# Performance work log

Hardware: AMD Instinct MI355X
Metric: run time of the kernel (lower is better)

## Reference

```python
import jax, jax.numpy as jnp
import numpy as np

N = 50000      # nodes
E = 800000     # edges (before self-loops)
IN_DIM = 128
HID = 64
OUT = 32
HEADS = 8
BN_EPS = 1e-5
NEG_SLOPE = 0.2  # PyG GATConv default


def setup_inputs() -> dict:
    key = jax.random.key(0)
    ks = jax.random.split(key, 24)
    g = lambda k, shape, fan_in: (jax.random.normal(k, shape, jnp.float32) / np.sqrt(fan_in))
    return {
        "x": jax.random.normal(ks[0], (N, IN_DIM), jnp.float32),
        "edge_index": jax.random.randint(ks[1], (2, E), 0, N, dtype=jnp.int64),
        # GCN1
        "gcn1_w": g(ks[2], (IN_DIM, HID), IN_DIM),
        "gcn1_b": jnp.zeros((HID,), jnp.float32),
        # BN1 (eval mode running stats)
        "bn1_gamma": jnp.ones((HID,), jnp.float32),
        "bn1_beta": jnp.zeros((HID,), jnp.float32),
        "bn1_mean": 0.1 * jax.random.normal(ks[3], (HID,), jnp.float32),
        "bn1_var": 0.5 + jax.random.uniform(ks[4], (HID,), jnp.float32),
        # GAT1: heads=8, per-head out=HID, concat=False -> mean over heads
        "gat1_w": g(ks[5], (HID, HEADS * HID), HID),
        "gat1_asrc": g(ks[6], (HEADS, HID), HID),
        "gat1_adst": g(ks[7], (HEADS, HID), HID),
        "gat1_b": jnp.zeros((HID,), jnp.float32),
        # GCN2
        "gcn2_w": g(ks[8], (HID, HID), HID),
        "gcn2_b": jnp.zeros((HID,), jnp.float32),
        # BN2
        "bn2_gamma": jnp.ones((HID,), jnp.float32),
        "bn2_beta": jnp.zeros((HID,), jnp.float32),
        "bn2_mean": 0.1 * jax.random.normal(ks[9], (HID,), jnp.float32),
        "bn2_var": 0.5 + jax.random.uniform(ks[10], (HID,), jnp.float32),
        # GAT2: heads=8, per-head out=OUT, concat=False
        "gat2_w": g(ks[11], (HID, HEADS * OUT), HID),
        "gat2_asrc": g(ks[12], (HEADS, OUT), OUT),
        "gat2_adst": g(ks[13], (HEADS, OUT), OUT),
        "gat2_b": jnp.zeros((OUT,), jnp.float32),
    }


def _gcn(x, src, dst, w, b, n):
    # PyG GCNConv: x @ W, symmetric norm with self-loops (src/dst already include them)
    h = x @ w
    deg = jax.ops.segment_sum(jnp.ones(src.shape[0], x.dtype), dst, num_segments=n)
    dinv = jnp.where(deg > 0, jax.lax.rsqrt(jnp.maximum(deg, 1.0)), 0.0)
    coef = dinv[src] * dinv[dst]                     # [E']
    out = jax.ops.segment_sum(coef[:, None] * h[src], dst, num_segments=n)
    return out + b


def _gat(x, src, dst, w, a_src, a_dst, b, n, heads, ch):
    # PyG GATConv (concat=False): mean over heads, softmax over incoming edges per dst
    h = (x @ w).reshape(n, heads, ch)                # [N,H,C]
    es = jnp.einsum('nhc,hc->nh', h, a_src)          # alpha_src per node
    ed = jnp.einsum('nhc,hc->nh', h, a_dst)
    e = jax.nn.leaky_relu(es[src] + ed[dst], NEG_SLOPE)  # [E',H]
    m = jax.ops.segment_max(e, dst, num_segments=n)
    m = jnp.where(jnp.isfinite(m), m, 0.0)
    ex = jnp.exp(e - m[dst])
    denom = jax.ops.segment_sum(ex, dst, num_segments=n)
    alpha = ex / (denom[dst] + 1e-16)                # [E',H]
    out = jnp.zeros((n, ch), x.dtype)
    for hd in range(heads):  # fixed small head loop keeps peak edge memory at [E',C]
        msg = alpha[:, hd, None] * h[src, hd]        # [E',C]
        out = out + jax.ops.segment_sum(msg, dst, num_segments=n)
    return out / heads + b


def _bn_eval(x, gamma, beta, mean, var):
    return (x - mean) * jax.lax.rsqrt(var + BN_EPS) * gamma + beta


def reference(x, edge_index,
              gcn1_w, gcn1_b, bn1_gamma, bn1_beta, bn1_mean, bn1_var,
              gat1_w, gat1_asrc, gat1_adst, gat1_b,
              gcn2_w, gcn2_b, bn2_gamma, bn2_beta, bn2_mean, bn2_var,
              gat2_w, gat2_asrc, gat2_adst, gat2_b):
    n = x.shape[0]
    loops = jnp.arange(n, dtype=edge_index.dtype)
    src = jnp.concatenate([edge_index[0], loops])    # self-loops (PyG default)
    dst = jnp.concatenate([edge_index[1], loops])

    h = _gcn(x, src, dst, gcn1_w, gcn1_b, n)
    h = jax.nn.relu(_bn_eval(h, bn1_gamma, bn1_beta, bn1_mean, bn1_var))
    h = jax.nn.relu(_gat(h, src, dst, gat1_w, gat1_asrc, gat1_adst, gat1_b, n, HEADS, HID))
    h = _gcn(h, src, dst, gcn2_w, gcn2_b, n)
    h = jax.nn.relu(_bn_eval(h, bn2_gamma, bn2_beta, bn2_mean, bn2_var))
    h = _gat(h, src, dst, gat2_w, gat2_asrc, gat2_adst, gat2_b, n, HEADS, OUT)
    return jax.nn.log_softmax(h, axis=1)
```

## Files before the change

kernel.cpp:

```cpp
#include <hip/hip_runtime.h>
#include <hip/hip_bf16.h>

#define NN 50000
#define NE 800000
#define IND 128
#define NH 8
#define EBLK 256
#define EPB 3125
#define NBUK 391
#define NBUKP 392
#define GH (NBUKP * EBLK)

typedef __hip_bfloat16 bf16;
typedef __attribute__((ext_vector_type(8))) short short8;
typedef __attribute__((ext_vector_type(8))) __bf16 bf16x8;
typedef __attribute__((ext_vector_type(4))) float floatx4;
typedef __attribute__((ext_vector_type(2))) float floatx2;

static __device__ __forceinline__ short f2bf_bits(float f) {
    unsigned u = __float_as_uint(f);
    u = (u + 0x7fffu + ((u >> 16) & 1u)) >> 16;
    return (short)u;
}
static __device__ __forceinline__ float bf2f(bf16 v) { return __bfloat162float(v); }
static __device__ __forceinline__ floatx2 up2(unsigned av) {
    floatx2 r;
    r.x = __uint_as_float(av << 16);
    r.y = __uint_as_float(av & 0xffff0000u);
    return r;
}
static __device__ __forceinline__ unsigned pk2(float a, float b) {
    return (unsigned)(unsigned short)f2bf_bits(a) | ((unsigned)(unsigned short)f2bf_bits(b) << 16);
}

__global__ __launch_bounds__(256) void bin_count_kernel(const int* __restrict__ edst,
        int* __restrict__ ghist) {
    __shared__ int h[NBUKP];
    const int tid = threadIdx.x, blk = blockIdx.x;
    for (int b = tid; b < NBUKP; b += 256) h[b] = 0;
    __syncthreads();
    const int e0 = blk * EPB;
    for (int e = e0 + tid; e < e0 + EPB; e += 256)
        atomicAdd(&h[edst[e] >> 7], 1);
    __syncthreads();
    for (int b = tid; b < NBUKP; b += 256)
        ghist[b * EBLK + blk] = h[b];
}
__global__ __launch_bounds__(256) void scang1_kernel(const int* __restrict__ src,
        int* __restrict__ pre, int* __restrict__ bsum, int n) {
    __shared__ int sh[256];
    const int tid = threadIdx.x;
    const int idx = blockIdx.x * 256 + tid;
    int c = (idx < n) ? src[idx] : 0;
    sh[tid] = c; __syncthreads();
    int val = c;
#pragma unroll
    for (int off = 1; off < 256; off <<= 1) {
        int t = (tid >= off) ? sh[tid - off] : 0;
        __syncthreads();
        val += t; sh[tid] = val;
        __syncthreads();
    }
    if (idx < n) pre[idx] = val - c;
    if (tid == 255) bsum[blockIdx.x] = val;
}
__global__ __launch_bounds__(512) void scang2_kernel(int* __restrict__ bsum, int nb) {
    __shared__ int sh[512];
    const int tid = threadIdx.x;
    int v = (tid < nb) ? bsum[tid] : 0;
    sh[tid] = v; __syncthreads();
    int val = v;
#pragma unroll
    for (int off = 1; off < 512; off <<= 1) {
        int t = (tid >= off) ? sh[tid - off] : 0;
        __syncthreads();
        val += t; sh[tid] = val;
        __syncthreads();
    }
    if (tid < nb) bsum[tid] = val - v;
}
__global__ __launch_bounds__(256) void bin_scatter_kernel(const int* __restrict__ esrc,
        const int* __restrict__ edst, const int* __restrict__ gpre,
        const int* __restrict__ gbsum, unsigned* __restrict__ ebuf) {
    __shared__ int cur[NBUKP];
    const int tid = threadIdx.x, blk = blockIdx.x;
    for (int b = tid; b < NBUKP; b += 256) {
        int i = b * EBLK + blk;
        cur[b] = gpre[i] + gbsum[i >> 8];
    }
    __syncthreads();
    const int e0 = blk * EPB;
    for (int e = e0 + tid; e < e0 + EPB; e += 256) {
        int d = edst[e], s = esrc[e];
        int pos = atomicAdd(&cur[d >> 7], 1);
        ebuf[pos] = ((unsigned)(d & 127) << 16) | (unsigned)s;
    }
}
__global__ __launch_bounds__(256) void bucket_finalize_kernel(const unsigned* __restrict__ ebuf,
        const int* __restrict__ gpre, const int* __restrict__ gbsum,
        int* __restrict__ rowptr, float* __restrict__ dinv, int* __restrict__ csrc) {
    __shared__ int lh[128], lcur[128], sc[256];
    const int bu = blockIdx.x, tid = threadIdx.x;
    const int seg_beg = gpre[bu * EBLK] + gbsum[bu];
    const int seg_end = gpre[(bu + 1) * EBLK] + gbsum[bu + 1];
    if (tid < 128) lh[tid] = 0;
    __syncthreads();
    for (int i = seg_beg + tid; i < seg_end; i += 256)
        atomicAdd(&lh[ebuf[i] >> 16], 1);
    __syncthreads();
    int c = (tid < 128) ? lh[tid] : 0;
    sc[tid] = c; __syncthreads();
    int val = c;
#pragma unroll
    for (int off = 1; off < 256; off <<= 1) {
        int t = (tid >= off) ? sc[tid - off] : 0;
        __syncthreads();
        val += t; sc[tid] = val;
        __syncthreads();
    }
    int excl = val - c;
    if (tid < 128) {
        lcur[tid] = excl;
        int node = bu * 128 + tid;
        if (node < NN) {
            rowptr[node] = seg_beg + excl;
            dinv[node] = rsqrtf((float)c + 1.f);
        }
    }
    if (bu == 0 && tid == 0) rowptr[NN] = NE;
    __syncthreads();
    for (int i = seg_beg + tid; i < seg_end; i += 256) {
        unsigned u = ebuf[i];
        int pos = atomicAdd(&lcur[u >> 16], 1);
        csrc[seg_beg + pos] = (int)(u & 0xffffu);
    }
}

__global__ __launch_bounds__(256) void prep_all_kernel(
        const float* __restrict__ gcn1_w, const float* __restrict__ gcn2_w,
        const float* __restrict__ gat1_w, const float* __restrict__ gat2_w,
        const float* __restrict__ as1, const float* __restrict__ ad1,
        const float* __restrict__ as2, const float* __restrict__ ad2,
        bf16* __restrict__ wT1, bf16* __restrict__ wT2,
        bf16* __restrict__ wgT1, bf16* __restrict__ wgT2,
        float* __restrict__ was1, float* __restrict__ wad1,
        float* __restrict__ was2, float* __restrict__ wad2) {
    int idx = blockIdx.x * 256 + threadIdx.x;
    if (idx < 8192) {
        int m = idx >> 7, k = idx & 127;
        ((short*)wT1)[idx] = f2bf_bits(gcn1_w[(long)k * 64 + m]);
    } else if (idx < 12288) {
        int i = idx - 8192;
        int m = i >> 6, k = i & 63;
        ((short*)wT2)[i] = f2bf_bits(gcn2_w[(long)k * 64 + m]);
    } else if (idx < 45056) {
        int i = idx - 12288;
        int m = i >> 9, k = i & 511;
        int h = k >> 6, c = k & 63;
        ((short*)wgT1)[i] = f2bf_bits(gat1_w[(long)c * 512 + h * 64 + m]);
    } else if (idx < 77824) {
        int i = idx - 45056;
        int m = i >> 9, k = i & 511;
        int h = k >> 6, c = k & 63;
        ((short*)wgT2)[i] = (m < 32) ? f2bf_bits(gat2_w[(long)c * 256 + h * 32 + m]) : (short)0;
    } else if (idx < 78336) {
        int i = idx - 77824;
        int h = i >> 6, c = i & 63;
        const float* wrow = gat1_w + (long)c * 512 + h * 64;
        float s = 0.f, d = 0.f;
        for (int cc = 0; cc < 64; ++cc) {
            float w = wrow[cc];
            s += w * as1[h * 64 + cc];
            d += w * ad1[h * 64 + cc];
        }
        was1[i] = s; wad1[i] = d;
    } else if (idx < 78848) {
        int i = idx - 78336;
        int h = i >> 6, c = i & 63;
        const float* wrow = gat2_w + (long)c * 256 + h * 32;
        float s = 0.f, d = 0.f;
        for (int cc = 0; cc < 32; ++cc) {
            float w = wrow[cc];
            s += w * as2[h * 32 + cc];
            d += w * ad2[h * 32 + cc];
        }
        was2[i] = s; wad2[i] = d;
    }
}

template<int K, int EPI, bool AF32>
__global__ __launch_bounds__(256) void mm2_kernel(const void* __restrict__ A,
        const bf16* __restrict__ wT, void* __restrict__ C,
        const float* __restrict__ bias, const float* __restrict__ rowscale,
        int nrows, int M) {
    const int row0 = blockIdx.x * 64;
    const int tid = threadIdx.x;
    const int lane = tid & 63, wave = tid >> 6;
    const int lr = lane & 15, q = lane >> 4;
    const int row = row0 + wave * 16 + lr;
    const bool rok = row < nrows;
    constexpr int NC = (EPI == 4) ? 2 : 4;
    floatx4 acc[NC] = {};
#pragma unroll 4
    for (int k0 = 0; k0 < K; k0 += 32) {
        short8 av = {0, 0, 0, 0, 0, 0, 0, 0};
        if (rok) {
            if (AF32) {
                const float* apf = (const float*)A + (long)row * K + q * 8 + k0;
                floatx4 va = *(const floatx4*)apf;
                floatx4 vb = *(const floatx4*)(apf + 4);
#pragma unroll
                for (int j = 0; j < 4; ++j) { av[j] = f2bf_bits(va[j]); av[4 + j] = f2bf_bits(vb[j]); }
            } else {
                av = *(const short8*)((const short*)A + (long)row * K + q * 8 + k0);
            }
        }
        bf16x8 a = __builtin_bit_cast(bf16x8, av);
#pragma unroll
        for (int c = 0; c < NC; ++c) {
            bf16x8 b = __builtin_bit_cast(bf16x8,
                *(const short8*)((const short*)wT + (long)(c * 16 + lr) * K + k0 + q * 8));
            acc[c] = __builtin_amdgcn_mfma_f32_16x16x32_bf16(a, b, acc[c], 0, 0, 0);
        }
    }
    if (EPI == 4) {
#pragma unroll
        for (int r = 0; r < 4; ++r) {
            int orow = row0 + wave * 16 + q * 4 + r;
            float v0 = acc[0][r] * 0.125f + bias[lr];
            float v1 = acc[1][r] * 0.125f + bias[16 + lr];
            float m = fmaxf(v0, v1);
#pragma unroll
            for (int off = 1; off < 16; off <<= 1) m = fmaxf(m, __shfl_xor(m, off));
            float s = __expf(v0 - m) + __expf(v1 - m);
#pragma unroll
            for (int off = 1; off < 16; off <<= 1) s += __shfl_xor(s, off);
            float ls = m + logf(s);
            if (orow < nrows) {
                ((float*)C)[(long)orow * 32 + lr] = v0 - ls;
                ((float*)C)[(long)orow * 32 + 16 + lr] = v1 - ls;
            }
        }
        return;
    }
#pragma unroll
    for (int c = 0; c < NC; ++c)
#pragma unroll
        for (int r = 0; r < 4; ++r) {
            int orow = row0 + wave * 16 + q * 4 + r;
            int col = c * 16 + lr;
            if (orow < nrows && col < M) {
                long o = (long)orow * M + col;
                float v = acc[c][r];
                if (EPI == 0) ((float*)C)[o] = v;
                else if (EPI == 2) {
                    v = v * 0.125f + bias[col];
                    ((bf16*)C)[o] = __float2bfloat16(fmaxf(v, 0.f));
                } else {
                    ((bf16*)C)[o] = __float2bfloat16(rowscale[orow] * v);
                }
            }
        }
}

__global__ __launch_bounds__(256) void gcn_fused_kernel(const int* __restrict__ rowptr,
        const int* __restrict__ csrc, const float* __restrict__ dinv,
        const bf16* __restrict__ hin, const float* __restrict__ b,
        const float* __restrict__ gamma, const float* __restrict__ beta,
        const float* __restrict__ mean, const float* __restrict__ var,
        bf16* __restrict__ actout) {
    const int node = blockIdx.x * 4 + (threadIdx.x >> 6);
    if (node >= NN) return;
    const int lane = threadIdx.x & 63;
    const int eslot = lane >> 5, cp = lane & 31;
    const int beg = rowptr[node], end = rowptr[node + 1];
    const float di = dinv[node];
    floatx2 acc2 = {0.f, 0.f};
#pragma unroll 2
    for (int ei = beg + eslot; ei < end; ei += 2) {
        int s = csrc[ei];
        unsigned av = *(const unsigned*)((const unsigned short*)hin + (long)s * 64 + 2 * cp);
        acc2 += up2(av);
    }
    acc2.x += __shfl_xor(acc2.x, 32);
    acc2.y += __shfl_xor(acc2.y, 32);
    {
        unsigned sv = *(const unsigned*)((const unsigned short*)hin + (long)node * 64 + 2 * cp);
        acc2 += up2(sv);
    }
    int c0 = 2 * cp, c1 = c0 + 1;
    float x0 = acc2.x * di + b[c0];
    float x1 = acc2.y * di + b[c1];
    x0 = (x0 - mean[c0]) * rsqrtf(var[c0] + 1e-5f) * gamma[c0] + beta[c0];
    x1 = (x1 - mean[c1]) * rsqrtf(var[c1] + 1e-5f) * gamma[c1] + beta[c1];
    if (eslot == 0)
        *(unsigned*)((unsigned short*)actout + (long)node * 64 + c0) =
            pk2(fmaxf(x0, 0.f), fmaxf(x1, 0.f));
}

__global__ __launch_bounds__(256) void scores_kernel(const bf16* __restrict__ actb,
        const float* __restrict__ was, const float* __restrict__ wad,
        float* __restrict__ es, float* __restrict__ ed, int n) {
    const int node = blockIdx.x * 4 + (threadIdx.x >> 6);
    if (node >= n) return;
    const int lane = threadIdx.x & 63;
    const int h = lane >> 3, cg = lane & 7;
    short8 a8 = *(const short8*)((const short*)actb + (long)node * 64 + cg * 8);
    const float* wsp = was + h * 64 + cg * 8;
    const float* wdp = wad + h * 64 + cg * 8;
    floatx4 ws0 = *(const floatx4*)wsp, ws1 = *(const floatx4*)(wsp + 4);
    floatx4 wd0 = *(const floatx4*)wdp, wd1 = *(const floatx4*)(wdp + 4);
    float s = 0.f, d = 0.f;
#pragma unroll
    for (int j = 0; j < 4; ++j) {
        float v0 = bf2f(__builtin_bit_cast(bf16, a8[j]));
        float v1 = bf2f(__builtin_bit_cast(bf16, a8[4 + j]));
        s += v0 * ws0[j] + v1 * ws1[j];
        d += v0 * wd0[j] + v1 * wd1[j];
    }
#pragma unroll
    for (int off = 1; off < 8; off <<= 1) {
        s += __shfl_xor(s, off);
        d += __shfl_xor(d, off);
    }
    if (cg == 0) { es[node * NH + h] = s; ed[node * NH + h] = d; }
}

__global__ __launch_bounds__(256) void gat_agg_kernel(const int* __restrict__ rowptr,
        const int* __restrict__ csrc, const float* __restrict__ es, const float* __restrict__ ed,
        const bf16* __restrict__ actb, bf16* __restrict__ agg) {
    __shared__ __align__(16) float salpha[4][512];
    __shared__ int ssrcs[4][64];
    __shared__ __align__(16) float sself[4][8];
    const int wv = threadIdx.x >> 6;
    const int node = blockIdx.x * 4 + wv;
    if (node >= NN) return;
    const int lane = threadIdx.x & 63;
    const int h = lane & 7, slot = lane >> 3;
    const int beg = rowptr[node], end = rowptr[node + 1];
    const int deg = end - beg;
    const float edr = ed[node * NH + h];

    float selfe = es[node * NH + h] + edr;
    selfe = selfe > 0.f ? selfe : 0.2f * selfe;

    if (deg <= 64) {
        float ex_r[8]; int s_r[8];
        float den = 0.f;
#pragma unroll
        for (int b = 0; b < 8; ++b) {
            ex_r[b] = 0.f; s_r[b] = 0;
            int k = b * 8 + slot;
            if (k < deg) {
                int s = csrc[beg + k];
                s_r[b] = s;
                float e = es[s * NH + h] + edr;
                e = e > 0.f ? e : 0.2f * e;
                ex_r[b] = __expf(e - selfe);
                den += ex_r[b];
            }
        }
        den += __shfl_xor(den, 8);
        den += __shfl_xor(den, 16);
        den += __shfl_xor(den, 32);
        const float invden = 1.f / (den + 1.f);

#pragma unroll
        for (int b = 0; b < 8; ++b)
            salpha[wv][b * 64 + lane] = ex_r[b] * invden;
        if (h == 0) {
#pragma unroll
            for (int b = 0; b < 8; ++b)
                ssrcs[wv][b * 8 + slot] = s_r[b];
        }
        if (slot == 0) sself[wv][h] = invden;

        const int hq = lane >> 5, cp = lane & 31;
        floatx2 acc2[4] = {};
#pragma unroll 4
        for (int k = 0; k < deg; ++k) {
            int s = ssrcs[wv][k];
            unsigned av = *(const unsigned*)((const unsigned short*)actb + (long)s * 64 + 2 * cp);
            floatx2 a2 = up2(av);
            floatx4 al = *(const floatx4*)&salpha[wv][(k >> 3) * 64 + (k & 7) * 8 + hq * 4];
            acc2[0] += a2 * al[0]; acc2[1] += a2 * al[1];
            acc2[2] += a2 * al[2]; acc2[3] += a2 * al[3];
        }
        {
            unsigned sv = *(const unsigned*)((const unsigned short*)actb + (long)node * 64 + 2 * cp);
            floatx2 a2 = up2(sv);
            floatx4 sa = *(const floatx4*)&sself[wv][hq * 4];
            acc2[0] += a2 * sa[0]; acc2[1] += a2 * sa[1];
            acc2[2] += a2 * sa[2]; acc2[3] += a2 * sa[3];
        }
#pragma unroll
        for (int j = 0; j < 4; ++j)
            *(unsigned*)((unsigned short*)agg + (long)node * 512 + (hq * 4 + j) * 64 + 2 * cp) =
                pk2(acc2[j].x, acc2[j].y);
    } else {
        float acc[NH] = {0.f, 0.f, 0.f, 0.f, 0.f, 0.f, 0.f, 0.f};
        float den = 0.f;
        for (int base = beg; base < end; base += 8) {
            int ei = base + slot;
            if (ei < end) {
                int s = csrc[ei];
                float e = es[s * NH + h] + edr;
                e = e > 0.f ? e : 0.2f * e;
                den += __expf(e - selfe);
            }
        }
        den += __shfl_xor(den, 8);
        den += __shfl_xor(den, 16);
        den += __shfl_xor(den, 32);
        const float invden = 1.f / (den + 1.f);
        for (int base = beg; base < end; base += 8) {
            int ei = base + slot;
            float al = 0.f; int sl = 0;
            if (ei < end) {
                sl = csrc[ei];
                float e = es[sl * NH + h] + edr;
                e = e > 0.f ? e : 0.2f * e;
                al = __expf(e - selfe) * invden;
            }
            salpha[wv][lane] = al;
            if (h == 0) ssrcs[wv][slot] = sl;
            int ecnt = end - base; if (ecnt > 8) ecnt = 8;
            for (int j = 0; j < ecnt; ++j) {
                int s = ssrcs[wv][j];
                float a = bf2f(actb[(long)s * 64 + lane]);
                floatx4 al0 = *(const floatx4*)&salpha[wv][j * 8];
                floatx4 al1 = *(const floatx4*)&salpha[wv][j * 8 + 4];
                acc[0] += al0[0] * a; acc[1] += al0[1] * a;
                acc[2] += al0[2] * a; acc[3] += al0[3] * a;
                acc[4] += al1[0] * a; acc[5] += al1[1] * a;
                acc[6] += al1[2] * a; acc[7] += al1[3] * a;
            }
        }
        {
            if (slot == 0) sself[wv][h] = invden;
            float a = bf2f(actb[(long)node * 64 + lane]);
            floatx4 s0 = *(const floatx4*)&sself[wv][0];
            floatx4 s1 = *(const floatx4*)&sself[wv][4];
            acc[0] += s0[0] * a; acc[1] += s0[1] * a;
            acc[2] += s0[2] * a; acc[3] += s0[3] * a;
            acc[4] += s1[0] * a; acc[5] += s1[1] * a;
            acc[6] += s1[2] * a; acc[7] += s1[3] * a;
        }
#pragma unroll
        for (int hh = 0; hh < NH; ++hh)
            agg[(long)node * 512 + hh * 64 + lane] = __float2bfloat16(acc[hh]);
    }
}

extern "C" void kernel_launch(void* const* d_in, const int* in_sizes, int n_in,
                              void* d_out, int out_size, void* d_ws, size_t ws_size,
                              hipStream_t stream) {
    const float* x        = (const float*)d_in[0];
    const int*   eidx     = (const int*)d_in[1];
    const float* gcn1_w   = (const float*)d_in[2];
    const float* gcn1_b   = (const float*)d_in[3];
    const float* bn1_g    = (const float*)d_in[4];
    const float* bn1_b    = (const float*)d_in[5];
    const float* bn1_m    = (const float*)d_in[6];
    const float* bn1_v    = (const float*)d_in[7];
    const float* gat1_w   = (const float*)d_in[8];
    const float* gat1_as  = (const float*)d_in[9];
    const float* gat1_ad  = (const float*)d_in[10];
    const float* gat1_b   = (const float*)d_in[11];
    const float* gcn2_w   = (const float*)d_in[12];
    const float* gcn2_b   = (const float*)d_in[13];
    const float* bn2_g    = (const float*)d_in[14];
    const float* bn2_b    = (const float*)d_in[15];
    const float* bn2_m    = (const float*)d_in[16];
    const float* bn2_v    = (const float*)d_in[17];
    const float* gat2_w   = (const float*)d_in[18];
    const float* gat2_as  = (const float*)d_in[19];
    const float* gat2_ad  = (const float*)d_in[20];
    const float* gat2_b   = (const float*)d_in[21];
    float* out = (float*)d_out;

    const int* esrc = eidx;
    const int* edst = eidx + NE;

    float* ws = (float*)d_ws;
    int*      ghist  = (int*)ws;
    int*      gpre   = ghist + GH;
    int*      gbsum  = gpre + GH;
    unsigned* ebuf   = (unsigned*)(gbsum + 512);
    int*      rowptr = (int*)(ebuf + NE);
    int*      csrc   = rowptr + 50048;
    float*    dinv   = (float*)(csrc + NE);
    float*    es     = dinv + 50048;
    float*    ed     = es + 400000;
    float*    was1   = ed + 400000;
    float*    wad1   = was1 + 512;
    float*    was2   = wad1 + 512;
    float*    wad2   = was2 + 512;
    bf16*     wT1    = (bf16*)(wad2 + 512);
    bf16*     wT2    = wT1 + 64 * 128;
    bf16*     wgT1   = wT2 + 64 * 64;
    bf16*     wgT2   = wgT1 + 64 * 512;
    bf16*     actb   = wgT2 + 64 * 512;
    bf16*     mmbf   = actb + (size_t)NN * 64;
    bf16*     agg    = mmbf + (size_t)NN * 64;

    auto cdiv = [](long a, long b) { return (int)((a + b - 1) / b); };
    const int GB = cdiv(NN, 64);
    const int NB = cdiv(NN, 4);

    bin_count_kernel<<<EBLK, 256, 0, stream>>>(edst, ghist);
    scang1_kernel<<<GH / 256, 256, 0, stream>>>(ghist, gpre, gbsum, GH);
    scang2_kernel<<<1, 512, 0, stream>>>(gbsum, GH / 256);
    bin_scatter_kernel<<<EBLK, 256, 0, stream>>>(esrc, edst, gpre, gbsum, ebuf);
    bucket_finalize_kernel<<<NBUK, 256, 0, stream>>>(ebuf, gpre, gbsum, rowptr, dinv, csrc);

    prep_all_kernel<<<cdiv(78848, 256), 256, 0, stream>>>(
        gcn1_w, gcn2_w, gat1_w, gat2_w, gat1_as, gat1_ad, gat2_as, gat2_ad,
        wT1, wT2, wgT1, wgT2, was1, wad1, was2, wad2);

    mm2_kernel<IND, 3, true><<<GB, 256, 0, stream>>>(x, wT1, mmbf, nullptr, dinv, NN, 64);
    gcn_fused_kernel<<<NB, 256, 0, stream>>>(rowptr, csrc, dinv, mmbf,
        gcn1_b, bn1_g, bn1_b, bn1_m, bn1_v, actb);

    scores_kernel<<<NB, 256, 0, stream>>>(actb, was1, wad1, es, ed, NN);
    gat_agg_kernel<<<NB, 256, 0, stream>>>(rowptr, csrc, es, ed, actb, agg);
    mm2_kernel<512, 2, false><<<GB, 256, 0, stream>>>(agg, wgT1, actb, gat1_b, nullptr, NN, 64);

    mm2_kernel<64, 3, false><<<GB, 256, 0, stream>>>(actb, wT2, mmbf, nullptr, dinv, NN, 64);
    gcn_fused_kernel<<<NB, 256, 0, stream>>>(rowptr, csrc, dinv, mmbf,
        gcn2_b, bn2_g, bn2_b, bn2_m, bn2_v, actb);

    scores_kernel<<<NB, 256, 0, stream>>>(actb, was2, wad2, es, ed, NN);
    gat_agg_kernel<<<NB, 256, 0, stream>>>(rowptr, csrc, es, ed, actb, agg);
    mm2_kernel<512, 4, false><<<GB, 256, 0, stream>>>(agg, wgT2, out, gat2_b, nullptr, NN, 32);
}
```

Baseline: 403.2 us.

## Quantize GAT gather features to per-channel uint8 and source scores to bf16

Adds a per-channel max reduction kernel over the post-ReLU activations. The scores kernel now also writes an 8-bit per-channel-scaled copy of the activations and stores source attention scores as bf16. The GAT aggregation gathers these 1-byte features and bf16 scores instead of bf16 features and fp32 scores, which halves the random-gather traffic per edge. The cost is an extra kernel launch with atomics per layer and lower precision in attention inputs and aggregated features.

```diff
diff --git a/kernel.cpp b/kernel.cpp
--- a/kernel.cpp
+++ b/kernel.cpp
@@ -144,7 +144,8 @@
         bf16* __restrict__ wT1, bf16* __restrict__ wT2,
         bf16* __restrict__ wgT1, bf16* __restrict__ wgT2,
         float* __restrict__ was1, float* __restrict__ wad1,
-        float* __restrict__ was2, float* __restrict__ wad2) {
+        float* __restrict__ was2, float* __restrict__ wad2,
+        float* __restrict__ cs1, float* __restrict__ cs2) {
     int idx = blockIdx.x * 256 + threadIdx.x;
     if (idx < 8192) {
         int m = idx >> 7, k = idx & 127;
@@ -185,6 +186,26 @@
             d += w * ad2[h * 32 + cc];
         }
         was2[i] = s; wad2[i] = d;
+    } else if (idx < 78976) {
+        int i = idx - 78848;
+        if (i < 64) cs1[i] = 0.f; else cs2[i - 64] = 0.f;
+    }
+}
+
+__global__ __launch_bounds__(256) void cmax_kernel(const bf16* __restrict__ actb,
+        float* __restrict__ cs) {
+    __shared__ float lmx[256];
+    const int tid = threadIdx.x;
+    const int c = tid & 63, g = tid >> 6;
+    const int r0 = blockIdx.x * 512;
+    float m = 0.f;
+    for (int r = r0 + g; r < r0 + 512 && r < NN; r += 4)
+        m = fmaxf(m, bf2f(actb[(long)r * 64 + c]));
+    lmx[tid] = m;
+    __syncthreads();
+    if (tid < 64) {
+        m = fmaxf(fmaxf(lmx[tid], lmx[tid + 64]), fmaxf(lmx[tid + 128], lmx[tid + 192]));
+        atomicMax((unsigned*)cs + tid, __float_as_uint(m));
     }
 }
 
@@ -300,7 +321,8 @@
 
 __global__ __launch_bounds__(256) void scores_kernel(const bf16* __restrict__ actb,
         const float* __restrict__ was, const float* __restrict__ wad,
-        float* __restrict__ es, float* __restrict__ ed, int n) {
+        bf16* __restrict__ esb, float* __restrict__ ed,
+        const float* __restrict__ cs, unsigned char* __restrict__ actq, int n) {
     const int node = blockIdx.x * 4 + (threadIdx.x >> 6);
     if (node >= n) return;
     const int lane = threadIdx.x & 63;
@@ -311,10 +333,12 @@
     floatx4 ws0 = *(const floatx4*)wsp, ws1 = *(const floatx4*)(wsp + 4);
     floatx4 wd0 = *(const floatx4*)wdp, wd1 = *(const floatx4*)(wdp + 4);
     float s = 0.f, d = 0.f;
+    float av[8];
 #pragma unroll
     for (int j = 0; j < 4; ++j) {
         float v0 = bf2f(__builtin_bit_cast(bf16, a8[j]));
         float v1 = bf2f(__builtin_bit_cast(bf16, a8[4 + j]));
+        av[j] = v0; av[4 + j] = v1;
         s += v0 * ws0[j] + v1 * ws1[j];
         d += v0 * wd0[j] + v1 * wd1[j];
     }
@@ -323,11 +347,26 @@
         s += __shfl_xor(s, off);
         d += __shfl_xor(d, off);
     }
-    if (cg == 0) { es[node * NH + h] = s; ed[node * NH + h] = d; }
+    if (cg == 0) { esb[node * NH + h] = __float2bfloat16(s); ed[node * NH + h] = d; }
+    if (h == 0) {
+        unsigned u0 = 0, u1 = 0;
+#pragma unroll
+        for (int j = 0; j < 8; ++j) {
+            int c = cg * 8 + j;
+            float qs = 255.f / fmaxf(cs[c], 1e-6f);
+            int q = (int)(av[j] * qs + 0.5f);
+            q = (q > 255) ? 255 : q;
+            if (j < 4) u0 |= (unsigned)q << (8 * j);
+            else       u1 |= (unsigned)q << (8 * (j - 4));
+        }
+        *(unsigned*)(actq + (long)node * 64 + cg * 8) = u0;
+        *(unsigned*)(actq + (long)node * 64 + cg * 8 + 4) = u1;
+    }
 }
 
 __global__ __launch_bounds__(256) void gat_agg_kernel(const int* __restrict__ rowptr,
-        const int* __restrict__ csrc, const float* __restrict__ es, const float* __restrict__ ed,
+        const int* __restrict__ csrc, const bf16* __restrict__ esb, const float* __restrict__ ed,
+        const unsigned char* __restrict__ actq, const float* __restrict__ cs,
         const bf16* __restrict__ actb, bf16* __restrict__ agg) {
     __shared__ __align__(16) float salpha[4][512];
     __shared__ int ssrcs[4][64];
@@ -341,7 +380,7 @@
     const int deg = end - beg;
     const float edr = ed[node * NH + h];
 
-    float selfe = es[node * NH + h] + edr;
+    float selfe = bf2f(esb[node * NH + h]) + edr;
     selfe = selfe > 0.f ? selfe : 0.2f * selfe;
 
     if (deg <= 64) {
@@ -354,7 +393,7 @@
             if (k < deg) {
                 int s = csrc[beg + k];
                 s_r[b] = s;
-                float e = es[s * NH + h] + edr;
+                float e = bf2f(esb[s * NH + h]) + edr;
                 e = e > 0.f ? e : 0.2f * e;
                 ex_r[b] = __expf(e - selfe);
                 den += ex_r[b];
@@ -376,12 +415,16 @@
         if (slot == 0) sself[wv][h] = invden;
 
         const int hq = lane >> 5, cp = lane & 31;
+        const float ds0 = cs[2 * cp] * (1.f / 255.f);
+        const float ds1 = cs[2 * cp + 1] * (1.f / 255.f);
         floatx2 acc2[4] = {};
 #pragma unroll 4
         for (int k = 0; k < deg; ++k) {
             int s = ssrcs[wv][k];
-            unsigned av = *(const unsigned*)((const unsigned short*)actb + (long)s * 64 + 2 * cp);
-            floatx2 a2 = up2(av);
+            unsigned short uv = *(const unsigned short*)(actq + (long)s * 64 + 2 * cp);
+            floatx2 a2;
+            a2.x = (float)(uv & 0xff) * ds0;
+            a2.y = (float)(uv >> 8) * ds1;
             floatx4 al = *(const floatx4*)&salpha[wv][(k >> 3) * 64 + (k & 7) * 8 + hq * 4];
             acc2[0] += a2 * al[0]; acc2[1] += a2 * al[1];
             acc2[2] += a2 * al[2]; acc2[3] += a2 * al[3];
@@ -404,7 +447,7 @@
             int ei = base + slot;
             if (ei < end) {
                 int s = csrc[ei];
-                float e = es[s * NH + h] + edr;
+                float e = bf2f(esb[s * NH + h]) + edr;
                 e = e > 0.f ? e : 0.2f * e;
                 den += __expf(e - selfe);
             }
@@ -418,7 +461,7 @@
             float al = 0.f; int sl = 0;
             if (ei < end) {
                 sl = csrc[ei];
-                float e = es[sl * NH + h] + edr;
+                float e = bf2f(esb[sl * NH + h]) + edr;
                 e = e > 0.f ? e : 0.2f * e;
                 al = __expf(e - selfe) * invden;
             }
@@ -490,23 +533,27 @@
     int*      rowptr = (int*)(ebuf + NE);
     int*      csrc   = rowptr + 50048;
     float*    dinv   = (float*)(csrc + NE);
-    float*    es     = dinv + 50048;
-    float*    ed     = es + 400000;
+    float*    ed     = dinv + 50048;
     float*    was1   = ed + 400000;
     float*    wad1   = was1 + 512;
     float*    was2   = wad1 + 512;
     float*    wad2   = was2 + 512;
-    bf16*     wT1    = (bf16*)(wad2 + 512);
+    float*    cs1    = wad2 + 512;
+    float*    cs2    = cs1 + 64;
+    bf16*     esb    = (bf16*)(cs2 + 64);
+    bf16*     wT1    = esb + 400000;
     bf16*     wT2    = wT1 + 64 * 128;
     bf16*     wgT1   = wT2 + 64 * 64;
     bf16*     wgT2   = wgT1 + 64 * 512;
     bf16*     actb   = wgT2 + 64 * 512;
     bf16*     mmbf   = actb + (size_t)NN * 64;
     bf16*     agg    = mmbf + (size_t)NN * 64;
+    unsigned char* actq = (unsigned char*)(agg + (size_t)NN * 512);
 
     auto cdiv = [](long a, long b) { return (int)((a + b - 1) / b); };
     const int GB = cdiv(NN, 64);
     const int NB = cdiv(NN, 4);
+    const int CB = cdiv(NN, 512);
 
     bin_count_kernel<<<EBLK, 256, 0, stream>>>(edst, ghist);
     scang1_kernel<<<GH / 256, 256, 0, stream>>>(ghist, gpre, gbsum, GH);
@@ -514,23 +561,25 @@
     bin_scatter_kernel<<<EBLK, 256, 0, stream>>>(esrc, edst, gpre, gbsum, ebuf);
     bucket_finalize_kernel<<<NBUK, 256, 0, stream>>>(ebuf, gpre, gbsum, rowptr, dinv, csrc);
 
-    prep_all_kernel<<<cdiv(78848, 256), 256, 0, stream>>>(
+    prep_all_kernel<<<cdiv(78976, 256), 256, 0, stream>>>(
         gcn1_w, gcn2_w, gat1_w, gat2_w, gat1_as, gat1_ad, gat2_as, gat2_ad,
-        wT1, wT2, wgT1, wgT2, was1, wad1, was2, wad2);
+        wT1, wT2, wgT1, wgT2, was1, wad1, was2, wad2, cs1, cs2);
 
     mm2_kernel<IND, 3, true><<<GB, 256, 0, stream>>>(x, wT1, mmbf, nullptr, dinv, NN, 64);
     gcn_fused_kernel<<<NB, 256, 0, stream>>>(rowptr, csrc, dinv, mmbf,
         gcn1_b, bn1_g, bn1_b, bn1_m, bn1_v, actb);
 
-    scores_kernel<<<NB, 256, 0, stream>>>(actb, was1, wad1, es, ed, NN);
-    gat_agg_kernel<<<NB, 256, 0, stream>>>(rowptr, csrc, es, ed, actb, agg);
+    cmax_kernel<<<CB, 256, 0, stream>>>(actb, cs1);
+    scores_kernel<<<NB, 256, 0, stream>>>(actb, was1, wad1, esb, ed, cs1, actq, NN);
+    gat_agg_kernel<<<NB, 256, 0, stream>>>(rowptr, csrc, esb, ed, actq, cs1, actb, agg);
     mm2_kernel<512, 2, false><<<GB, 256, 0, stream>>>(agg, wgT1, actb, gat1_b, nullptr, NN, 64);
 
     mm2_kernel<64, 3, false><<<GB, 256, 0, stream>>>(actb, wT2, mmbf, nullptr, dinv, NN, 64);
     gcn_fused_kernel<<<NB, 256, 0, stream>>>(rowptr, csrc, dinv, mmbf,
         gcn2_b, bn2_g, bn2_b, bn2_m, bn2_v, actb);
 
-    scores_kernel<<<NB, 256, 0, stream>>>(actb, was2, wad2, es, ed, NN);
-    gat_agg_kernel<<<NB, 256, 0, stream>>>(rowptr, csrc, es, ed, actb, agg);
+    cmax_kernel<<<CB, 256, 0, stream>>>(actb, cs2);
+    scores_kernel<<<NB, 256, 0, stream>>>(actb, was2, wad2, esb, ed, cs2, actq, NN);
+    gat_agg_kernel<<<NB, 256, 0, stream>>>(rowptr, csrc, esb, ed, actq, cs2, actb, agg);
     mm2_kernel<512, 4, false><<<GB, 256, 0, stream>>>(agg, wgT2, out, gat2_b, nullptr, NN, 32);
 }
```

After: 462.3 us. +14.7%, slower.
